# Performance work log

Measured on AMD Instinct MI355X. Metric: run time of the kernel, lower is better.

The kernel has to match this reference:

```python
import jax, jax.numpy as jnp
import numpy as np

# SpecAugment hyperparameters (match init_kwargs)
FREQ_MASKS, MIN_FREQ, MAX_FREQ = 2, 0, 27
TIME_MASKS, MIN_TIME, MAX_TIME = 10, 0, 100


def setup_inputs() -> dict:
    key = jax.random.key(0)
    x = jax.random.normal(key, (128, 80, 4000), dtype=jnp.float32)
    return {"x": x}


def _band_mask(key, batch, dim, n_masks, wmin, wmax):
    """Vectorized equivalent of the per-sample randint loops.

    For each (sample, mask): width w ~ U{wmin..wmax}, start f0 ~ U{0..max(1, dim-w)-1},
    mask positions [f0, f0+w). Returns bool [batch, dim].
    """
    kw, ks = jax.random.split(key)
    w = jax.random.randint(kw, (batch, n_masks), wmin, wmax + 1)  # [B, M]
    hi = jnp.maximum(1, dim - w)                                   # per-mask start range
    start = jnp.floor(jax.random.uniform(ks, (batch, n_masks)) * hi).astype(jnp.int32)
    idx = jnp.arange(dim)                                          # [dim]
    # [B, M, dim]: inside [start, start+w)
    inside = (idx[None, None, :] >= start[..., None]) & (idx[None, None, :] < (start + w)[..., None])
    return jnp.any(inside, axis=1)                                 # [B, dim]


def reference(x):
    B, F, T = x.shape
    kf, kt = jax.random.split(jax.random.key(42))
    freq_mask = _band_mask(kf, B, F, FREQ_MASKS, MIN_FREQ, MAX_FREQ)  # [B, F]
    time_mask = _band_mask(kt, B, T, TIME_MASKS, MIN_TIME, MAX_TIME)  # [B, T]
    mask = freq_mask[:, :, None] | time_mask[:, None, :]              # [B, F, T]
    return jnp.where(mask, jnp.zeros((), x.dtype), x)
```

## Files before the change

kernel.cpp:

```cpp
#include <hip/hip_runtime.h>
#include <stdint.h>
#include <math.h>


#define BATCH 128
#define FREQ  80
#define TIME  4000
#define NTOT  (40960000u)

__device__ __forceinline__ uint2 tf2x32(uint32_t k0, uint32_t k1, uint32_t c0, uint32_t c1) {
  uint32_t ks0 = k0, ks1 = k1, ks2 = 0x1BD11BDAu ^ k0 ^ k1;
  uint32_t x0 = c0 + ks0, x1 = c1 + ks1;
#define TF_RND(r) { x0 += x1; x1 = (x1 << (r)) | (x1 >> (32 - (r))); x1 ^= x0; }
  TF_RND(13) TF_RND(15) TF_RND(26) TF_RND(6)
  x0 += ks1; x1 += ks2 + 1u;
  TF_RND(17) TF_RND(29) TF_RND(16) TF_RND(24)
  x0 += ks2; x1 += ks0 + 2u;
  TF_RND(13) TF_RND(15) TF_RND(26) TF_RND(6)
  x0 += ks0; x1 += ks1 + 3u;
  TF_RND(17) TF_RND(29) TF_RND(16) TF_RND(24)
  x0 += ks1; x1 += ks2 + 4u;
  TF_RND(13) TF_RND(15) TF_RND(26) TF_RND(6)
  x0 += ks2; x1 += ks0 + 5u;
#undef TF_RND
  return make_uint2(x0, x1);
}

__device__ __forceinline__ uint2 split_child(uint2 key, int i, bool part) {
  if (part) {
    return tf2x32(key.x, key.y, 0u, (uint32_t)i);
  }
  uint2 A = tf2x32(key.x, key.y, 0u, 2u);
  uint2 B = tf2x32(key.x, key.y, 1u, 3u);
  return (i == 0) ? make_uint2(A.x, B.x) : make_uint2(A.y, B.y);
}

__device__ __forceinline__ uint32_t bits32(uint2 key, uint32_t j, uint32_t n, bool part) {
  if (part) {
    uint2 r = tf2x32(key.x, key.y, 0u, j);
    return r.x ^ r.y;
  }
  uint32_t half = n >> 1;
  if (j < half) return tf2x32(key.x, key.y, j, j + half).x;
  return tf2x32(key.x, key.y, j - half, j).y;
}

__device__ __forceinline__ float u01(uint32_t b) {
  return __uint_as_float((b >> 9) | 0x3f800000u) - 1.0f;
}

__device__ __forceinline__ float hyp_x(uint32_t j, bool part) {
  uint32_t b = bits32(make_uint2(0u, 0u), j, NTOT, part);
  const float lo = -0.99999994f;
  float u = u01(b) * (1.0f - lo) + lo;
  if (u < lo) u = lo;
  return 1.41421356237f * erfinvf(u);
}

template <uint32_t SPAN, uint32_t MULT, int DIM, int M>
__device__ __forceinline__ void band_interval(uint2 kbranch, int b, int m, bool part,
                                              int* s_out, int* e_out) {
  uint2 kw = split_child(kbranch, 0, part);
  uint2 ks = split_child(kbranch, 1, part);
  uint2 k1 = split_child(kw, 0, part);
  uint2 k2 = split_child(kw, 1, part);
  const uint32_t BM = (uint32_t)(BATCH * M);
  const uint32_t j = (uint32_t)(b * M + m);
  uint32_t h = bits32(k1, j, BM, part);
  uint32_t l = bits32(k2, j, BM, part);
  uint32_t w = ((h % SPAN) * MULT + (l % SPAN)) % SPAN;
  uint32_t ub = bits32(ks, j, BM, part);
  float u = u01(ub);
  int hi = DIM - (int)w;
  if (hi < 1) hi = 1;
  int start = (int)floorf(u * (float)hi);
  *s_out = start;
  *e_out = start + (int)w;
}

__global__ __launch_bounds__(256) void specaug_kernel(const float* __restrict__ x,
                                                      float* __restrict__ out) {
  __shared__ int s_fs[2], s_fe[2];
  __shared__ int s_ts[10], s_te[10];
  __shared__ int s_part;

  const int row = blockIdx.x;
  const int b = row / FREQ;
  const int f = row - b * FREQ;
  const int tid = threadIdx.x;

  if (tid == 0) {
    int vp = 0, vl = 0;
    for (uint32_t j = 0; j < 4; ++j) {
      float xv = x[j];
      float tol = 1e-3f * (1.0f + fabsf(xv));
      vp += (fabsf(hyp_x(j, true) - xv) < tol);
      vl += (fabsf(hyp_x(j, false) - xv) < tol);
    }
    s_part = (vl >= 3 && vp < 3) ? 0 : 1;
  }
  __syncthreads();
  const bool part = (s_part != 0);

  if (tid < 12) {
    uint2 kf = split_child(make_uint2(0u, 42u), 0, part);
    uint2 kt = split_child(make_uint2(0u, 42u), 1, part);
    if (tid < 2) {
      band_interval<28u, 4u, FREQ, 2>(kf, b, tid, part, &s_fs[tid], &s_fe[tid]);
    } else {
      int m = tid - 2;
      band_interval<101u, 68u, TIME, 10>(kt, b, m, part, &s_ts[m], &s_te[m]);
    }
  }
  __syncthreads();

  const bool row_masked = (f >= s_fs[0] && f < s_fe[0]) || (f >= s_fs[1] && f < s_fe[1]);

  const float4* __restrict__ xr = (const float4*)(x + ((size_t)row) * TIME);
  float4* __restrict__ orow = (float4*)(out + ((size_t)row) * TIME);

  if (row_masked) {
    const float4 z = make_float4(0.f, 0.f, 0.f, 0.f);
    for (int i = tid; i < TIME / 4; i += 256) orow[i] = z;
  } else {
    for (int i = tid; i < TIME / 4; i += 256) {
      float4 v = xr[i];
      const int t0 = i * 4;
      bool m0 = false, m1 = false, m2 = false, m3 = false;
#pragma unroll
      for (int k = 0; k < 10; k++) {
        const int s = s_ts[k], e = s_te[k];
        m0 |= (t0 >= s) & (t0 < e);
        m1 |= (t0 + 1 >= s) & (t0 + 1 < e);
        m2 |= (t0 + 2 >= s) & (t0 + 2 < e);
        m3 |= (t0 + 3 >= s) & (t0 + 3 < e);
      }
      if (m0) v.x = 0.f;
      if (m1) v.y = 0.f;
      if (m2) v.z = 0.f;
      if (m3) v.w = 0.f;
      orow[i] = v;
    }
  }
}

extern "C" void kernel_launch(void* const* d_in, const int* in_sizes, int n_in,
                              void* d_out, int out_size, void* d_ws, size_t ws_size,
                              hipStream_t stream) {
  (void)in_sizes; (void)n_in; (void)d_ws; (void)ws_size; (void)out_size;
  const float* x = (const float*)d_in[0];
  float* out = (float*)d_out;
  specaug_kernel<<<dim3(BATCH * FREQ), dim3(256), 0, stream>>>(x, out);
}
```

Before: 280.2 us.

## Precompute band masks once per sample and stream rows with bitmask lookup

Moves the per-row RNG work (probe and Threefry band generation) out of the streaming loop. A small setup kernel now writes the per-sample frequency intervals and a time bitmask to workspace, and a persistent grid-stride kernel applies them. A fused fallback for when no workspace is available makes each block handle five rows with a shared-memory bitmask. The aim is to cut redundant RNG computation across the 10240 blocks and replace the 10-interval compare per element with a bit lookup, at the cost of an extra launch and a dependence between the two kernels.

```diff
diff --git a/kernel.cpp b/kernel.cpp
--- a/kernel.cpp
+++ b/kernel.cpp
@@ -7,6 +7,11 @@
 #define FREQ  80
 #define TIME  4000
 #define NTOT  (40960000u)
+#define ROWS  (BATCH * FREQ)
+#define TM_WORDS  125
+#define TM_STRIDE 128
+#define WS_FREQ_WORDS (BATCH * 4)
+#define WS_NEEDED ((size_t)(WS_FREQ_WORDS + BATCH * TM_STRIDE) * 4)
 
 __device__ __forceinline__ uint2 tf2x32(uint32_t k0, uint32_t k1, uint32_t c0, uint32_t c1) {
   uint32_t ks0 = k0, ks1 = k1, ks2 = 0x1BD11BDAu ^ k0 ^ k1;
@@ -78,29 +83,114 @@
   *e_out = start + (int)w;
 }
 
-__global__ __launch_bounds__(256) void specaug_kernel(const float* __restrict__ x,
-                                                      float* __restrict__ out) {
+__device__ __forceinline__ void probe_fill(const float* __restrict__ x, int tid, int* s_m) {
+  if (tid < 8) {
+    bool p = (tid < 4);
+    uint32_t j = (uint32_t)(tid & 3);
+    float xv = x[j];
+    float tol = 1e-3f * (1.0f + fabsf(xv));
+    s_m[tid] = (fabsf(hyp_x(j, p) - xv) < tol) ? 1 : 0;
+  }
+}
+__device__ __forceinline__ bool probe_decide(const int* s_m) {
+  int vp = s_m[0] + s_m[1] + s_m[2] + s_m[3];
+  int vl = s_m[4] + s_m[5] + s_m[6] + s_m[7];
+  return !(vl >= 3 && vp < 3);
+}
+
+__device__ __forceinline__ uint32_t paint_word(int word, const int* s_ts, const int* s_te) {
+  const int base = word * 32;
+  uint32_t wm = 0u;
+#pragma unroll
+  for (int k = 0; k < 10; k++) {
+    int lo = s_ts[k] - base;
+    int hi = s_te[k] - base;
+    lo = lo < 0 ? 0 : lo;
+    hi = hi > 32 ? 32 : hi;
+    if (hi > lo) {
+      uint32_t mh = (hi == 32) ? 0xffffffffu : ((1u << hi) - 1u);
+      wm |= mh & ~((1u << lo) - 1u);
+    }
+  }
+  return wm;
+}
+
+__global__ __launch_bounds__(128) void setup_kernel(const float* __restrict__ x,
+                                                    uint32_t* __restrict__ ws) {
+  __shared__ int s_m[8];
+  __shared__ int s_ts[10], s_te[10];
+  const int b = blockIdx.x;
+  const int tid = threadIdx.x;
+
+  probe_fill(x, tid, s_m);
+  __syncthreads();
+  const bool part = probe_decide(s_m);
+
+  if (tid < 12) {
+    uint2 kf = split_child(make_uint2(0u, 42u), 0, part);
+    uint2 kt = split_child(make_uint2(0u, 42u), 1, part);
+    if (tid < 2) {
+      int s, e;
+      band_interval<28u, 4u, FREQ, 2>(kf, b, tid, part, &s, &e);
+      ((int*)ws)[b * 4 + tid * 2]     = s;
+      ((int*)ws)[b * 4 + tid * 2 + 1] = e;
+    } else {
+      int m = tid - 2, s, e;
+      band_interval<101u, 68u, TIME, 10>(kt, b, m, part, &s, &e);
+      s_ts[m] = s; s_te[m] = e;
+    }
+  }
+  __syncthreads();
+
+  if (tid < TM_WORDS) {
+    ws[WS_FREQ_WORDS + b * TM_STRIDE + tid] = paint_word(tid, s_ts, s_te);
+  }
+}
+
+__global__ __launch_bounds__(256) void stream_kernel(const float* __restrict__ x,
+                                                     float* __restrict__ out,
+                                                     const uint32_t* __restrict__ ws) {
+  const int tid = threadIdx.x;
+  for (int row = blockIdx.x; row < ROWS; row += gridDim.x) {
+    const int b = row / FREQ;
+    const int f = row - b * FREQ;
+    const int4 fi = ((const int4*)ws)[b];
+    const bool row_masked = (f >= fi.x && f < fi.y) || (f >= fi.z && f < fi.w);
+
+    const float4* __restrict__ xr = (const float4*)(x + (size_t)row * TIME);
+    float4* __restrict__ orow = (float4*)(out + (size_t)row * TIME);
+
+    if (row_masked) {
+      const float4 z = make_float4(0.f, 0.f, 0.f, 0.f);
+      for (int i = tid; i < TIME / 4; i += 256) orow[i] = z;
+    } else {
+      const uint32_t* __restrict__ tm = ws + WS_FREQ_WORDS + b * TM_STRIDE;
+      for (int i = tid; i < TIME / 4; i += 256) {
+        float4 v = xr[i];
+        const uint32_t nib = (tm[i >> 3] >> ((i & 7) << 2)) & 0xFu;
+        if (nib & 1u) v.x = 0.f;
+        if (nib & 2u) v.y = 0.f;
+        if (nib & 4u) v.z = 0.f;
+        if (nib & 8u) v.w = 0.f;
+        orow[i] = v;
+      }
+    }
+  }
+}
+
+__global__ __launch_bounds__(256) void fused_kernel(const float* __restrict__ x,
+                                                    float* __restrict__ out) {
+  __shared__ int s_m[8];
   __shared__ int s_fs[2], s_fe[2];
   __shared__ int s_ts[10], s_te[10];
-  __shared__ int s_part;
-
-  const int row = blockIdx.x;
-  const int b = row / FREQ;
-  const int f = row - b * FREQ;
+  __shared__ uint32_t s_tm[TM_WORDS];
   const int tid = threadIdx.x;
-
-  if (tid == 0) {
-    int vp = 0, vl = 0;
-    for (uint32_t j = 0; j < 4; ++j) {
-      float xv = x[j];
-      float tol = 1e-3f * (1.0f + fabsf(xv));
-      vp += (fabsf(hyp_x(j, true) - xv) < tol);
-      vl += (fabsf(hyp_x(j, false) - xv) < tol);
-    }
-    s_part = (vl >= 3 && vp < 3) ? 0 : 1;
-  }
-  __syncthreads();
-  const bool part = (s_part != 0);
+  const int b  = blockIdx.x >> 4;
+  const int fg = (blockIdx.x & 15) * 5;
+
+  probe_fill(x, tid, s_m);
+  __syncthreads();
+  const bool part = probe_decide(s_m);
 
   if (tid < 12) {
     uint2 kf = split_child(make_uint2(0u, 42u), 0, part);
@@ -113,33 +203,28 @@
     }
   }
   __syncthreads();
-
-  const bool row_masked = (f >= s_fs[0] && f < s_fe[0]) || (f >= s_fs[1] && f < s_fe[1]);
-
-  const float4* __restrict__ xr = (const float4*)(x + ((size_t)row) * TIME);
-  float4* __restrict__ orow = (float4*)(out + ((size_t)row) * TIME);
-
-  if (row_masked) {
-    const float4 z = make_float4(0.f, 0.f, 0.f, 0.f);
-    for (int i = tid; i < TIME / 4; i += 256) orow[i] = z;
-  } else {
-    for (int i = tid; i < TIME / 4; i += 256) {
-      float4 v = xr[i];
-      const int t0 = i * 4;
-      bool m0 = false, m1 = false, m2 = false, m3 = false;
-#pragma unroll
-      for (int k = 0; k < 10; k++) {
-        const int s = s_ts[k], e = s_te[k];
-        m0 |= (t0 >= s) & (t0 < e);
-        m1 |= (t0 + 1 >= s) & (t0 + 1 < e);
-        m2 |= (t0 + 2 >= s) & (t0 + 2 < e);
-        m3 |= (t0 + 3 >= s) & (t0 + 3 < e);
+  if (tid < TM_WORDS) s_tm[tid] = paint_word(tid, s_ts, s_te);
+  __syncthreads();
+
+  for (int fo = 0; fo < 5; ++fo) {
+    const int f = fg + fo;
+    const int row = b * FREQ + f;
+    const bool row_masked = (f >= s_fs[0] && f < s_fe[0]) || (f >= s_fs[1] && f < s_fe[1]);
+    const float4* __restrict__ xr = (const float4*)(x + (size_t)row * TIME);
+    float4* __restrict__ orow = (float4*)(out + (size_t)row * TIME);
+    if (row_masked) {
+      const float4 z = make_float4(0.f, 0.f, 0.f, 0.f);
+      for (int i = tid; i < TIME / 4; i += 256) orow[i] = z;
+    } else {
+      for (int i = tid; i < TIME / 4; i += 256) {
+        float4 v = xr[i];
+        const uint32_t nib = (s_tm[i >> 3] >> ((i & 7) << 2)) & 0xFu;
+        if (nib & 1u) v.x = 0.f;
+        if (nib & 2u) v.y = 0.f;
+        if (nib & 4u) v.z = 0.f;
+        if (nib & 8u) v.w = 0.f;
+        orow[i] = v;
       }
-      if (m0) v.x = 0.f;
-      if (m1) v.y = 0.f;
-      if (m2) v.z = 0.f;
-      if (m3) v.w = 0.f;
-      orow[i] = v;
     }
   }
 }
@@ -147,8 +232,13 @@
 extern "C" void kernel_launch(void* const* d_in, const int* in_sizes, int n_in,
                               void* d_out, int out_size, void* d_ws, size_t ws_size,
                               hipStream_t stream) {
-  (void)in_sizes; (void)n_in; (void)d_ws; (void)ws_size; (void)out_size;
+  (void)in_sizes; (void)n_in; (void)out_size;
   const float* x = (const float*)d_in[0];
   float* out = (float*)d_out;
-  specaug_kernel<<<dim3(BATCH * FREQ), dim3(256), 0, stream>>>(x, out);
-}
+  if (d_ws != nullptr && ws_size >= WS_NEEDED) {
+    setup_kernel<<<dim3(BATCH), dim3(128), 0, stream>>>(x, (uint32_t*)d_ws);
+    stream_kernel<<<dim3(2048), dim3(256), 0, stream>>>(x, out, (const uint32_t*)d_ws);
+  } else {
+    fused_kernel<<<dim3(2048), dim3(256), 0, stream>>>(x, out);
+  }
+}
```

After: 279.2 us. Within noise of the previous version (-0.3%).
